# Kernel tuning notes

Measured on AMD Instinct MI355X. Metric: run time of the kernel, lower is better.

## Reference

```python
import jax, jax.numpy as jnp
import numpy as np

LN_EPS = 1e-5  # torch.nn.LayerNorm default

def g(x):
    # minGRU activation: x + 0.5 for x >= 0, sigmoid(x) otherwise (always positive)
    return jnp.where(x >= 0, x + 0.5, jax.nn.sigmoid(x))

def log_g(x):
    return jnp.where(x >= 0, jnp.log(jax.nn.relu(x) + 0.5), -jax.nn.softplus(-x))

def layernorm(x, gamma, beta):
    mu = jnp.mean(x, axis=-1, keepdims=True)
    var = jnp.var(x, axis=-1, keepdims=True)
    return (x - mu) * jax.lax.rsqrt(var + LN_EPS) * gamma + beta

def mingru_scan(gate, hidden, h0):
    # gate, hidden: (B,S,D); h0: (B,1,D) positive
    # z = sigmoid(gate); h_t = (1-z_t)*h_{t-1} + z_t * g(hidden_t)
    # evaluated via Heinsen parallel scan in log space
    log_z = -jax.nn.softplus(-gate)          # log sigmoid(gate)
    log_coeffs = -jax.nn.softplus(gate)      # log(1 - sigmoid(gate))
    log_h0 = jnp.log(h0)                     # (B,1,D)
    log_tilde_h = log_g(hidden)
    a_star = jnp.cumsum(
        jnp.concatenate([jnp.zeros_like(log_h0), log_coeffs], axis=1), axis=1
    )                                        # (B,S+1,D)
    log_vals = jnp.concatenate([log_h0, log_z + log_tilde_h], axis=1) - a_star
    log_h = a_star + jax.lax.cumlogsumexp(log_vals, axis=1)
    return jnp.exp(log_h)[:, 1:]             # (B,S,D)

def setup_inputs() -> dict:
    key = jax.random.key(0)
    k1, k2 = jax.random.split(key)
    B, S, D, L = 8, 4096, 1024, 3
    x = jax.random.normal(k1, (B, S, D), dtype=jnp.float32)
    W = jax.random.normal(k2, (L, D, 2 * D), dtype=jnp.float32) * 0.02
    b = jnp.zeros((L, 2 * D), dtype=jnp.float32)
    ln_gamma = jnp.ones((L, D), dtype=jnp.float32)
    ln_beta = jnp.zeros((L, D), dtype=jnp.float32)
    return {"x": x, "ln_gamma": ln_gamma, "ln_beta": ln_beta, "W": W, "b": b}

def reference(x, ln_gamma, ln_beta, W, b):
    B, S, D = x.shape
    L = W.shape[0]
    inp = x
    next_hidden = []
    for l in range(L):
        h_prev = jnp.full((B, 1, D), 0.5, dtype=x.dtype)  # g(zeros) = 0.5
        xn = layernorm(inp, ln_gamma[l], ln_beta[l])
        gh = jnp.einsum('bsd,de->bse', xn, W[l]) + b[l]   # (B,S,2D)
        gate, hidden = jnp.split(gh, 2, axis=2)
        out = mingru_scan(gate, hidden, h_prev)
        next_hidden.append(out[:, -1:])
        out = out + inp  # residual (sizes equal -> identity res_align)
        inp = out
    return (out, *next_hidden)
```

## Files before the change

### kernel.cpp

```cpp
#include <hip/hip_runtime.h>

typedef unsigned short u16;
typedef unsigned int   u32;
typedef float  f32x2  __attribute__((ext_vector_type(2)));
typedef float  f32x4  __attribute__((ext_vector_type(4)));
typedef short  bf16x8 __attribute__((ext_vector_type(8)));
typedef u16    u16x4  __attribute__((ext_vector_type(4)));
typedef u32    u32x4  __attribute__((ext_vector_type(4)));

#define BQ 8
#define SQ 4096
#define DQ 1024
#define NQ 2048
#define MQ 32768
#define KQ 1024
#define CCH 128
#define TCH 32
#define NT 16

__device__ __forceinline__ float bf2f(u16 u){
  union { u32 i; float f; } v; v.i = ((u32)u) << 16; return v.f;
}
__device__ __forceinline__ u16 f2bf(float f){
  union { float f; u32 i; } v; v.f = f;
  u32 r = v.i + 0x7fffu + ((v.i >> 16) & 1u);
  return (u16)(r >> 16);
}

__device__ __forceinline__ void sig_ab(float gate, float hid, float& a, float& bv){
  float eg = __expf(gate);
  float a_ = __builtin_amdgcn_rcpf(1.f + eg);
  float z  = 1.f - a_;
  float eh = __expf(hid);
  float sg = eh * __builtin_amdgcn_rcpf(1.f + eh);
  float gval = (hid >= 0.f) ? (hid + 0.5f) : sg;
  a = a_; bv = z * gval;
}

__device__ __forceinline__ void gload_lds16(const u16* g, u16* l){
  __builtin_amdgcn_global_load_lds(
      (const __attribute__((address_space(1))) u32*)g,
      (__attribute__((address_space(3)))       u32*)l,
      16, 0, 0);
}

__global__ __launch_bounds__(256) void wt_cast(const float* __restrict__ W,
                                               u16* __restrict__ WT){
  __shared__ float t[64][65];
  const int l  = blockIdx.z;
  const int k0 = blockIdx.x << 6, n0 = blockIdx.y << 6;
  const float* Wl = W  + (size_t)l * KQ * NQ;
  u16*         Tl = WT + (size_t)l * NQ * KQ;
  const int c = threadIdx.x & 63, r4 = threadIdx.x >> 6;
  #pragma unroll
  for (int i = 0; i < 16; ++i){
    int r = i * 4 + r4;
    t[r][c] = Wl[(size_t)(k0 + r) * NQ + n0 + c];
  }
  __syncthreads();
  #pragma unroll
  for (int i = 0; i < 16; ++i){
    int r = i * 4 + r4;
    const int n = n0 + r;
    const int d = n & 1023, ishid = n >> 10;
    const int np = ((d >> 4) << 5) + (ishid << 4) + (d & 15);
    Tl[(size_t)np * KQ + k0 + c] = f2bf(t[c][r]);
  }
}

__global__ __launch_bounds__(256) void ln_cast(const float* __restrict__ x,
                                               const float* __restrict__ gamma,
                                               const float* __restrict__ beta,
                                               u16* __restrict__ xn){
  const size_t row = blockIdx.x;
  const int tid = threadIdx.x;
  f32x4 xv = *(const f32x4*)(x + row * DQ + tid * 4);
  float s  = xv[0] + xv[1] + xv[2] + xv[3];
  float s2 = xv[0]*xv[0] + xv[1]*xv[1] + xv[2]*xv[2] + xv[3]*xv[3];
  #pragma unroll
  for (int off = 32; off > 0; off >>= 1){
    s  += __shfl_down(s,  off);
    s2 += __shfl_down(s2, off);
  }
  __shared__ float red[8];
  const int wave = tid >> 6, lane = tid & 63;
  if (lane == 0){ red[wave] = s; red[4 + wave] = s2; }
  __syncthreads();
  s  = red[0] + red[1] + red[2] + red[3];
  s2 = red[4] + red[5] + red[6] + red[7];
  const float mean = s * (1.f / DQ);
  float var = fmaxf(s2 * (1.f / DQ) - mean * mean, 0.f);
  const float rstd = rsqrtf(var + 1e-5f);
  f32x4 gv = *(const f32x4*)(gamma + tid * 4);
  f32x4 bv = *(const f32x4*)(beta  + tid * 4);
  u16x4 o;
  #pragma unroll
  for (int e = 0; e < 4; ++e) o[e] = f2bf((xv[e] - mean) * rstd * gv[e] + bv[e]);
  *(u16x4*)(xn + row * DQ + tid * 4) = o;
}

__global__ __launch_bounds__(256, 2) void gemm_k2(const u16* __restrict__ A,
                                                  const u16* __restrict__ Bt,
                                                  const float* __restrict__ bias,
                                                  u32* __restrict__ abv,
                                                  float* __restrict__ pq){
  __shared__ u16 lds[2][2][2][4096];
  const int bid = blockIdx.x;
  const int swz = ((bid & 7) << 9) | (bid >> 3);
  const int bn = swz & 15, bm = swz >> 4;
  const int m0 = bm << 7;
  const int tid = threadIdx.x;
  const int w = tid >> 6, lane = tid & 63;
  const int wr = w >> 1, wc = w & 1;
  const int lr = lane & 15, hi = lane >> 4;
  const int sw = (hi ^ ((lr >> 1) & 3)) << 4;

  f32x4 acc[4][4] = {};
  bf16x8 af[4], bf[4];

#define FENCE asm volatile("" ::: "memory")
#define BAR do { FENCE; __builtin_amdgcn_s_barrier(); FENCE; } while(0)

#define STAGE(op, kh, kt, pb_) do {                                            \
    const u16* gsrc_ = (op) ? Bt : A;                                          \
    const int rb_ = (op) ? (bn << 7) : m0;                                     \
    _Pragma("unroll")                                                          \
    for (int g_ = 0; g_ < 2; ++g_){                                            \
      const int row_ = (g_ << 6) + (tid >> 2);                                 \
      const int gs_  = ((tid & 3) ^ ((row_ >> 1) & 3)) << 3;                   \
      gload_lds16(gsrc_ + (size_t)(rb_ + row_) * KQ + ((kt) << 6) +            \
                      ((kh) << 5) + gs_,                                       \
                  &lds[pb_][op][kh][(g_ << 11) + (w << 9)]);                   \
    }                                                                          \
  } while(0)

#define RD_A(kh, buf_) do {                                                    \
    const char* Ah_ = (const char*)&lds[buf_][0][kh][0];                       \
    _Pragma("unroll")                                                          \
    for (int i_ = 0; i_ < 4; ++i_)                                             \
      af[i_] = *(const bf16x8*)(Ah_ + (((wr << 6) + (i_ << 4) + lr) << 6) + sw);\
  } while(0)

#define RD_B(kh, buf_) do {                                                    \
    const char* Bh_ = (const char*)&lds[buf_][1][kh][0];                       \
    _Pragma("unroll")                                                          \
    for (int j_ = 0; j_ < 4; ++j_)                                             \
      bf[j_] = *(const bf16x8*)(Bh_ + (((wc << 6) + (j_ << 4) + lr) << 6) + sw);\
  } while(0)

#define MM do {                                                                \
    __builtin_amdgcn_s_setprio(1);                                             \
    _Pragma("unroll")                                                          \
    for (int i_ = 0; i_ < 4; ++i_)                                             \
      _Pragma("unroll")                                                        \
      for (int j_ = 0; j_ < 4; ++j_)                                           \
        acc[i_][j_] = __builtin_amdgcn_mfma_f32_16x16x32_bf16(                 \
            af[i_], bf[j_], acc[i_][j_], 0, 0, 0);                             \
    __builtin_amdgcn_s_setprio(0);                                             \
  } while(0)

  STAGE(0, 0, 0, 0); STAGE(0, 1, 0, 0); STAGE(1, 0, 0, 0); STAGE(1, 1, 0, 0);

  for (int t = 0; t < NT; ++t){
    const int pb = t & 1, qb = pb ^ 1;
    const bool s = (t + 1 < NT);
    asm volatile("s_waitcnt vmcnt(2)" ::: "memory");
    BAR;
    if (s){ STAGE(0, 0, t + 1, qb); STAGE(0, 1, t + 1, qb); }
    RD_A(0, pb); RD_B(0, pb);
    MM;
    if (s) { asm volatile("s_waitcnt vmcnt(4)" ::: "memory"); }
    else   { asm volatile("s_waitcnt vmcnt(0)" ::: "memory"); }
    BAR;
    if (s){ STAGE(1, 0, t + 1, qb); STAGE(1, 1, t + 1, qb); }
    RD_A(1, pb); RD_B(1, pb);
    MM;
  }
#undef MM
#undef RD_B
#undef RD_A
#undef STAGE

  const int dbase = (bn << 6) + (wc << 5) + lr;
  float bg[2], bh[2];
  #pragma unroll
  for (int jp = 0; jp < 2; ++jp){
    bg[jp] = bias[dbase + (jp << 4)];
    bh[jp] = bias[1024 + dbase + (jp << 4)];
  }
  const int row00 = m0 + (wr << 6);
  #pragma unroll
  for (int half = 0; half < 2; ++half){
    float chP[2] = {1.f, 1.f}, chQ[2] = {0.f, 0.f};
    #pragma unroll
    for (int ii = 0; ii < 2; ++ii){
      const int i = (half << 1) + ii;
      float sgP[2] = {1.f, 1.f}, sgQ[2] = {0.f, 0.f};
      #pragma unroll
      for (int r = 0; r < 4; ++r){
        const int row = row00 + (i << 4) + (hi << 2) + r;
        #pragma unroll
        for (int jp = 0; jp < 2; ++jp){
          const int d = dbase + (jp << 4);
          float gate = acc[i][jp << 1][r]       + bg[jp];
          float hid  = acc[i][(jp << 1) + 1][r] + bh[jp];
          float a, bv; sig_ab(gate, hid, a, bv);
          u32 pk;
          asm volatile("v_cvt_pk_bf16_f32 %0, %1, %2"
                       : "=v"(pk) : "v"(a), "v"(bv));
          abv[(size_t)row * 1024 + d] = pk;
          union { u32 u; float f; } ua, ub;
          ua.u = pk << 16; ub.u = pk & 0xffff0000u;
          sgQ[jp] = ua.f * sgQ[jp] + ub.f;
          sgP[jp] *= ua.f;
        }
      }
      #pragma unroll
      for (int jp = 0; jp < 2; ++jp){
        float p = sgP[jp], q = sgQ[jp];
        float p1 = __shfl_up(p, 16), q1 = __shfl_up(q, 16);
        if (hi >= 1){ q = p * q1 + q; p = p * p1; }
        float p2 = __shfl_up(p, 32), q2 = __shfl_up(q, 32);
        if (hi >= 2){ q = p * q2 + q; p = p * p2; }
        chQ[jp] = p * chQ[jp] + q;
        chP[jp] = p * chP[jp];
      }
    }
    if (hi == 3){
      const int rowb = row00 + (half << 5);
      const int bq = rowb >> 12, cq = (rowb >> 5) & (CCH - 1);
      #pragma unroll
      for (int jp = 0; jp < 2; ++jp){
        const int d = dbase + (jp << 4);
        f32x2 v; v[0] = chP[jp]; v[1] = chQ[jp];
        *(f32x2*)(pq + ((((size_t)(bq * CCH + cq)) << 10) + d) * 2) = v;
      }
    }
  }
#undef BAR
#undef FENCE
}

__global__ __launch_bounds__(256) void scan2(const float* __restrict__ pq,
                                             float* __restrict__ hst,
                                             float* __restrict__ hlast){
  const int idx = blockIdx.x * 256 + threadIdx.x;
  const int b = idx >> 10, d = idx & 1023;
  float h = 0.5f;
  for (int c = 0; c < CCH; ++c){
    const size_t o = ((size_t)(b * CCH + c) << 10) + d;
    hst[o] = h;
    f32x2 v = *(const f32x2*)(pq + o * 2);
    h = v[0] * h + v[1];
  }
  hlast[idx] = h;
}

template<int MODE>
__global__ __launch_bounds__(256) void scan3f(const u32* __restrict__ abv,
                                              const float* __restrict__ hst,
                                              const void* __restrict__ inp,
                                              void* __restrict__ outp,
                                              u16* __restrict__ xn,
                                              const float* __restrict__ gamma,
                                              const float* __restrict__ beta){
  const int b = blockIdx.x >> 7;
  const int c = blockIdx.x & (CCH - 1);
  const int tid = threadIdx.x;
  const int d4 = tid << 2;
  const int wave = tid >> 6, lane = tid & 63;
  const size_t srow = (size_t)b * SQ + (size_t)c * TCH;
  const u32* base = abv + srow * 1024 + d4;
  const size_t o = ((size_t)blockIdx.x << 10) + d4;
  f32x4 h0v = *(const f32x4*)(hst + o);
  float h[4] = {h0v[0], h0v[1], h0v[2], h0v[3]};
  __shared__ float red[2][8];
  f32x4 gv = {}, bvv = {};
  if (MODE != 2){
    gv  = *(const f32x4*)(gamma + d4);
    bvv = *(const f32x4*)(beta  + d4);
  }
  for (int t = 0; t < TCH; ++t){
    u32x4 ab = *(const u32x4*)(base + (size_t)t * 1024);
    f32x4 iv;
    if (MODE == 0){
      iv = *(const f32x4*)((const float*)inp + (srow + t) * DQ + d4);
    } else {
      u16x4 ib = *(const u16x4*)((const u16*)inp + (srow + t) * DQ + d4);
      #pragma unroll
      for (int e = 0; e < 4; ++e) iv[e] = bf2f(ib[e]);
    }
    f32x4 ov;
    #pragma unroll
    for (int e = 0; e < 4; ++e){
      const float a  = bf2f((u16)(ab[e] & 0xffffu));
      const float bv = bf2f((u16)(ab[e] >> 16));
      h[e] = a * h[e] + bv;
      ov[e] = h[e] + iv[e];
    }
    if (MODE == 2){
      *(f32x4*)((float*)outp + (srow + t) * DQ + d4) = ov;
    } else {
      u16x4 ob;
      #pragma unroll
      for (int e = 0; e < 4; ++e) ob[e] = f2bf(ov[e]);
      *(u16x4*)((u16*)outp + (srow + t) * DQ + d4) = ob;
      float s  = ov[0] + ov[1] + ov[2] + ov[3];
      float s2 = ov[0]*ov[0] + ov[1]*ov[1] + ov[2]*ov[2] + ov[3]*ov[3];
      #pragma unroll
      for (int off = 32; off > 0; off >>= 1){
        s  += __shfl_down(s,  off);
        s2 += __shfl_down(s2, off);
      }
      const int rb = t & 1;
      if (lane == 0){ red[rb][wave] = s; red[rb][4 + wave] = s2; }
      __syncthreads();
      s  = red[rb][0] + red[rb][1] + red[rb][2] + red[rb][3];
      s2 = red[rb][4] + red[rb][5] + red[rb][6] + red[rb][7];
      const float mean = s * (1.f / DQ);
      float var = fmaxf(s2 * (1.f / DQ) - mean * mean, 0.f);
      const float rstd = rsqrtf(var + 1e-5f);
      u16x4 xo;
      #pragma unroll
      for (int e = 0; e < 4; ++e)
        xo[e] = f2bf((ov[e] - mean) * rstd * gv[e] + bvv[e]);
      *(u16x4*)(xn + (srow + t) * DQ + d4) = xo;
    }
  }
}

extern "C" void kernel_launch(void* const* d_in, const int* in_sizes, int n_in,
                              void* d_out, int out_size, void* d_ws, size_t ws_size,
                              hipStream_t stream) {
  const float* x     = (const float*)d_in[0];
  const float* gamma = (const float*)d_in[1];
  const float* beta  = (const float*)d_in[2];
  const float* W     = (const float*)d_in[3];
  const float* bias  = (const float*)d_in[4];
  float* out = (float*)d_out;

  char* ws = (char*)d_ws;
  const size_t ACT = (size_t)MQ * DQ * 4;
  u16*   bufA = (u16*)(ws);
  u16*   bufB = (u16*)(ws + ACT);
  u32*   abv  = (u32*)(ws + 2 * ACT);
  u16*   xn   = (u16*)(ws + 3 * ACT);
  u16*   WT   = (u16*)(ws + 3 * ACT + (size_t)MQ * DQ * 2);
  float* pq   = (float*)(ws + 3 * ACT + (size_t)MQ * DQ * 2 + (size_t)3 * NQ * KQ * 2);
  float* hst  = pq + (size_t)2 * BQ * CCH * DQ;

  wt_cast<<<dim3(KQ / 64, NQ / 64, 3), 256, 0, stream>>>(W, WT);

  const dim3 ggrid(16 * (MQ / 128));
  ln_cast<<<MQ, 256, 0, stream>>>(x, gamma, beta, xn);
  gemm_k2<<<ggrid, 256, 0, stream>>>(xn, WT, bias, abv, pq);
  scan2<<<(BQ * DQ) / 256, 256, 0, stream>>>(pq, hst, out + (size_t)MQ * DQ);
  scan3f<0><<<BQ * CCH, 256, 0, stream>>>(abv, hst, x, bufA, xn,
                                          gamma + DQ, beta + DQ);
  gemm_k2<<<ggrid, 256, 0, stream>>>(xn, WT + (size_t)NQ * KQ, bias + NQ,
                                     abv, pq);
  scan2<<<(BQ * DQ) / 256, 256, 0, stream>>>(pq, hst,
                                             out + (size_t)MQ * DQ + BQ * DQ);
  scan3f<1><<<BQ * CCH, 256, 0, stream>>>(abv, hst, bufA, bufB, xn,
                                          gamma + 2 * DQ, beta + 2 * DQ);
  gemm_k2<<<ggrid, 256, 0, stream>>>(xn, WT + (size_t)2 * NQ * KQ, bias + 2 * NQ,
                                     abv, pq);
  scan2<<<(BQ * DQ) / 256, 256, 0, stream>>>(pq, hst,
                                             out + (size_t)MQ * DQ + 2 * BQ * DQ);
  scan3f<2><<<BQ * CCH, 256, 0, stream>>>(abv, hst, bufB, out, nullptr,
                                          nullptr, nullptr);
}
```

Baseline: 806.6 us.

## Widen GEMM tile to 128x256 with 8 waves and single-stage K32 pipeline

Replaces the 128x128-tile, 4-wave GEMM with a 128x256-tile (128 gate/hidden pairs), 8-wave kernel, halving the grid. The K loop now steps in 32-wide slices with one barrier per iteration instead of two 32-wide halves per 64-wide step. The intent is better reuse of the A tile and fewer total loads per FLOP. The trade-off is a full vmcnt(0) wait each iteration, which exposes more load latency, and launch bounds of 512 threads with 4 blocks requested, which may cap registers.

```diff
diff --git a/kernel.cpp b/kernel.cpp
--- a/kernel.cpp
+++ b/kernel.cpp
@@ -16,7 +16,7 @@
 #define KQ 1024
 #define CCH 128
 #define TCH 32
-#define NT 16
+#define NT2 32
 
 __device__ __forceinline__ float bf2f(u16 u){
   union { u32 i; float f; } v; v.i = ((u32)u) << 16; return v.f;
@@ -99,21 +99,22 @@
   *(u16x4*)(xn + row * DQ + tid * 4) = o;
 }
 
-__global__ __launch_bounds__(256, 2) void gemm_k2(const u16* __restrict__ A,
+__global__ __launch_bounds__(512, 4) void gemm_t2(const u16* __restrict__ A,
                                                   const u16* __restrict__ Bt,
                                                   const float* __restrict__ bias,
                                                   u32* __restrict__ abv,
                                                   float* __restrict__ pq){
-  __shared__ u16 lds[2][2][2][4096];
+  __shared__ u16 lds[2][12288];
   const int bid = blockIdx.x;
-  const int swz = ((bid & 7) << 9) | (bid >> 3);
-  const int bn = swz & 15, bm = swz >> 4;
+  const int swz = ((bid & 7) << 8) | (bid >> 3);
+  const int bn = swz & 7, bm = swz >> 3;
   const int m0 = bm << 7;
   const int tid = threadIdx.x;
   const int w = tid >> 6, lane = tid & 63;
-  const int wr = w >> 1, wc = w & 1;
+  const int wr = w >> 2, wc = w & 3;
   const int lr = lane & 15, hi = lane >> 4;
-  const int sw = (hi ^ ((lr >> 1) & 3)) << 4;
+  const int srow = tid >> 2;
+  const int sslot = (tid & 3) ^ ((srow >> 1) & 3);
 
   f32x4 acc[4][4] = {};
   bf16x8 af[4], bf[4];
@@ -121,31 +122,34 @@
 #define FENCE asm volatile("" ::: "memory")
 #define BAR do { FENCE; __builtin_amdgcn_s_barrier(); FENCE; } while(0)
 
-#define STAGE(op, kh, kt, pb_) do {                                            \
-    const u16* gsrc_ = (op) ? Bt : A;                                          \
-    const int rb_ = (op) ? (bn << 7) : m0;                                     \
+#define STAGE(kt, pb_) do {                                                    \
+    gload_lds16(A + (size_t)(m0 + srow) * KQ + ((kt) << 5) + (sslot << 3),     \
+                &lds[pb_][w << 9]);                                            \
     _Pragma("unroll")                                                          \
     for (int g_ = 0; g_ < 2; ++g_){                                            \
-      const int row_ = (g_ << 6) + (tid >> 2);                                 \
-      const int gs_  = ((tid & 3) ^ ((row_ >> 1) & 3)) << 3;                   \
-      gload_lds16(gsrc_ + (size_t)(rb_ + row_) * KQ + ((kt) << 6) +            \
-                      ((kh) << 5) + gs_,                                       \
-                  &lds[pb_][op][kh][(g_ << 11) + (w << 9)]);                   \
+      const int row_ = (g_ << 7) + srow;                                       \
+      const int gs_  = (tid & 3) ^ ((row_ >> 1) & 3);                          \
+      gload_lds16(Bt + (size_t)((bn << 8) + row_) * KQ + ((kt) << 5) + (gs_ << 3),\
+                  &lds[pb_][4096 + (g_ << 12) + (w << 9)]);                    \
     }                                                                          \
   } while(0)
 
-#define RD_A(kh, buf_) do {                                                    \
-    const char* Ah_ = (const char*)&lds[buf_][0][kh][0];                       \
+#define RD_A(buf_) do {                                                        \
+    const char* Ah_ = (const char*)&lds[buf_][0];                              \
     _Pragma("unroll")                                                          \
-    for (int i_ = 0; i_ < 4; ++i_)                                             \
-      af[i_] = *(const bf16x8*)(Ah_ + (((wr << 6) + (i_ << 4) + lr) << 6) + sw);\
+    for (int i_ = 0; i_ < 4; ++i_){                                            \
+      const int r_ = (wr << 6) + (i_ << 4) + lr;                               \
+      af[i_] = *(const bf16x8*)(Ah_ + (r_ << 6) + ((hi ^ ((r_ >> 1) & 3)) << 4));\
+    }                                                                          \
   } while(0)
 
-#define RD_B(kh, buf_) do {                                                    \
-    const char* Bh_ = (const char*)&lds[buf_][1][kh][0];                       \
+#define RD_B(buf_) do {                                                        \
+    const char* Bh_ = (const char*)&lds[buf_][4096];                           \
     _Pragma("unroll")                                                          \
-    for (int j_ = 0; j_ < 4; ++j_)                                             \
-      bf[j_] = *(const bf16x8*)(Bh_ + (((wc << 6) + (j_ << 4) + lr) << 6) + sw);\
+    for (int j_ = 0; j_ < 4; ++j_){                                            \
+      const int r_ = (wc << 6) + (j_ << 4) + lr;                               \
+      bf[j_] = *(const bf16x8*)(Bh_ + (r_ << 6) + ((hi ^ ((r_ >> 1) & 3)) << 4));\
+    }                                                                          \
   } while(0)
 
 #define MM do {                                                                \
@@ -159,21 +163,14 @@
     __builtin_amdgcn_s_setprio(0);                                             \
   } while(0)
 
-  STAGE(0, 0, 0, 0); STAGE(0, 1, 0, 0); STAGE(1, 0, 0, 0); STAGE(1, 1, 0, 0);
-
-  for (int t = 0; t < NT; ++t){
+  STAGE(0, 0);
+
+  for (int t = 0; t < NT2; ++t){
     const int pb = t & 1, qb = pb ^ 1;
-    const bool s = (t + 1 < NT);
-    asm volatile("s_waitcnt vmcnt(2)" ::: "memory");
+    asm volatile("s_waitcnt vmcnt(0)" ::: "memory");
     BAR;
-    if (s){ STAGE(0, 0, t + 1, qb); STAGE(0, 1, t + 1, qb); }
-    RD_A(0, pb); RD_B(0, pb);
-    MM;
-    if (s) { asm volatile("s_waitcnt vmcnt(4)" ::: "memory"); }
-    else   { asm volatile("s_waitcnt vmcnt(0)" ::: "memory"); }
-    BAR;
-    if (s){ STAGE(1, 0, t + 1, qb); STAGE(1, 1, t + 1, qb); }
-    RD_A(1, pb); RD_B(1, pb);
+    if (t + 1 < NT2) STAGE(t + 1, qb);
+    RD_A(pb); RD_B(pb);
     MM;
   }
 #undef MM
@@ -181,7 +178,7 @@
 #undef RD_A
 #undef STAGE
 
-  const int dbase = (bn << 6) + (wc << 5) + lr;
+  const int dbase = (bn << 7) + (wc << 5) + lr;
   float bg[2], bh[2];
   #pragma unroll
   for (int jp = 0; jp < 2; ++jp){
@@ -351,19 +348,19 @@
 
   wt_cast<<<dim3(KQ / 64, NQ / 64, 3), 256, 0, stream>>>(W, WT);
 
-  const dim3 ggrid(16 * (MQ / 128));
+  const dim3 ggrid(8 * (MQ / 128));
   ln_cast<<<MQ, 256, 0, stream>>>(x, gamma, beta, xn);
-  gemm_k2<<<ggrid, 256, 0, stream>>>(xn, WT, bias, abv, pq);
+  gemm_t2<<<ggrid, 512, 0, stream>>>(xn, WT, bias, abv, pq);
   scan2<<<(BQ * DQ) / 256, 256, 0, stream>>>(pq, hst, out + (size_t)MQ * DQ);
   scan3f<0><<<BQ * CCH, 256, 0, stream>>>(abv, hst, x, bufA, xn,
                                           gamma + DQ, beta + DQ);
-  gemm_k2<<<ggrid, 256, 0, stream>>>(xn, WT + (size_t)NQ * KQ, bias + NQ,
+  gemm_t2<<<ggrid, 512, 0, stream>>>(xn, WT + (size_t)NQ * KQ, bias + NQ,
                                      abv, pq);
   scan2<<<(BQ * DQ) / 256, 256, 0, stream>>>(pq, hst,
                                              out + (size_t)MQ * DQ + BQ * DQ);
   scan3f<1><<<BQ * CCH, 256, 0, stream>>>(abv, hst, bufA, bufB, xn,
                                           gamma + 2 * DQ, beta + 2 * DQ);
-  gemm_k2<<<ggrid, 256, 0, stream>>>(xn, WT + (size_t)2 * NQ * KQ, bias + 2 * NQ,
+  gemm_t2<<<ggrid, 512, 0, stream>>>(xn, WT + (size_t)2 * NQ * KQ, bias + 2 * NQ,
                                      abv, pq);
   scan2<<<(BQ * DQ) / 256, 256, 0, stream>>>(pq, hst,
                                              out + (size_t)MQ * DQ + 2 * BQ * DQ);
```

New measurement: 743.2 us. -7.9%, faster.
